# Performance work log

Measured on AMD Instinct MI355X. Metric: run time of the kernel, lower is better.

The kernel has to match this reference:

```python
import jax, jax.numpy as jnp
from jax import lax
import numpy as np

B, S, D, H2, V = 1024, 256, 128, 5, 50257
EPS = 1e-5


def setup_inputs() -> dict:
    key = jax.random.key(0)
    ks = jax.random.split(key, 12)
    s = 0.08  # init scale ~ 1/sqrt(D)
    return {
        "x": jax.random.randint(ks[0], (B, S), 0, V),
        "emb": jax.random.normal(ks[1], (V, D), jnp.float32) * s,
        "W_ih1": jax.random.normal(ks[2], (D, D), jnp.float32) * s,
        "b_ih1": jax.random.normal(ks[3], (D,), jnp.float32) * s,
        "W_hh1": jax.random.normal(ks[4], (D, D), jnp.float32) * s,
        "b_hh1": jax.random.normal(ks[5], (D,), jnp.float32) * s,
        "g1": jnp.ones((D,), jnp.float32),
        "be1": jnp.zeros((D,), jnp.float32),
        "W_ih2": jax.random.normal(ks[6], (H2, D), jnp.float32) * s,
        "b_ih2": jax.random.normal(ks[7], (H2,), jnp.float32) * s,
        "W_hh2": jax.random.normal(ks[8], (H2, H2), jnp.float32) * s,
        "b_hh2": jax.random.normal(ks[9], (H2,), jnp.float32) * s,
        "g2": jnp.ones((H2,), jnp.float32),
        "be2": jnp.zeros((H2,), jnp.float32),
    }


def _rnn(xproj, W_hh):
    """Vanilla tanh RNN. xproj: [B,S,H] = x @ W_ih^T + b_ih + b_hh (precomputed)."""
    h0 = jnp.zeros((xproj.shape[0], W_hh.shape[0]), xproj.dtype)

    def step(h, xt):  # xt: [B,H]
        h = jnp.tanh(xt + h @ W_hh.T)
        return h, h

    _, hs = lax.scan(step, h0, jnp.swapaxes(xproj, 0, 1))  # [S,B,H]
    return jnp.swapaxes(hs, 0, 1)  # [B,S,H]


def _ln(z, g, b):
    m = jnp.mean(z, axis=-1, keepdims=True)
    v = jnp.mean(jnp.square(z - m), axis=-1, keepdims=True)
    return (z - m) * lax.rsqrt(v + EPS) * g + b


def reference(x, emb, W_ih1, b_ih1, W_hh1, b_hh1, g1, be1,
              W_ih2, b_ih2, W_hh2, b_hh2, g2, be2):
    e = emb[x]  # [B,S,D]
    z = _rnn(e @ W_ih1.T + (b_ih1 + b_hh1), W_hh1)
    z = _ln(z, g1, be1)
    z = _rnn(z @ W_ih2.T + (b_ih2 + b_hh2), W_hh2)  # [B,S,5]
    z = _ln(z, g2, be2)
    pooled = jnp.mean(z, axis=1)  # AvgPool1d over full seq -> [B,5]
    return jax.nn.softmax(pooled, axis=1)
```

## Files before the change

### kernel.cpp

```cpp
#include <hip/hip_runtime.h>
#include <stdint.h>

#define S_LEN 256
#define DIM   128
#define EPSL  1e-5f

typedef __bf16 bf16x8 __attribute__((ext_vector_type(8)));
typedef float  f32x4  __attribute__((ext_vector_type(4)));

__device__ __forceinline__ unsigned short f2bf_bits(float f) {
  union { float f; unsigned int u; } v; v.f = f;
  unsigned int r = v.u + 0x7fffu + ((v.u >> 16) & 1u);
  return (unsigned short)(r >> 16);
}
__device__ __forceinline__ float bf2f_bits(unsigned short b) {
  union { float f; unsigned int u; } v; v.u = ((unsigned int)b) << 16; return v.f;
}
__device__ __forceinline__ unsigned f2bf_rhu(float f) {
  return (__float_as_uint(f) + 0x8000u) >> 16;
}
__device__ __forceinline__ unsigned pack_rhu(float lo, float hi) {
  return __builtin_amdgcn_perm(__float_as_uint(hi) + 0x8000u,
                               __float_as_uint(lo) + 0x8000u, 0x07060302u);
}
__device__ __forceinline__ float tanh_fast(float x) {
  float e = __expf(2.f * x);
  return 1.f - 2.f * __builtin_amdgcn_rcpf(e + 1.f);
}

template<int CTRL>
__device__ __forceinline__ float dpp_rot_add(float v) {
  int r = __builtin_amdgcn_update_dpp(0, __float_as_int(v), CTRL, 0xF, 0xF, true);
  return v + __int_as_float(r);
}
template<int CTRL>
__device__ __forceinline__ float dpp_rot_max(float v) {
  int r = __builtin_amdgcn_update_dpp(0, __float_as_int(v), CTRL, 0xF, 0xF, true);
  return fmaxf(v, __int_as_float(r));
}
__device__ __forceinline__ float dpp_sum16(float v) {
  v = dpp_rot_add<0x124>(v); v = dpp_rot_add<0x128>(v);
  v = dpp_rot_add<0x39>(v);  v = dpp_rot_add<0x4E>(v);
  return v;
}
__device__ __forceinline__ float dpp_max16(float v) {
  v = dpp_rot_max<0x124>(v); v = dpp_rot_max<0x128>(v);
  v = dpp_rot_max<0x39>(v);  v = dpp_rot_max<0x4E>(v);
  return v;
}
template<int CTRL>
__device__ __forceinline__ void red_level7(float& s, float& sq, float* d) {
  s  = dpp_rot_add<CTRL>(s);
  sq = dpp_rot_add<CTRL>(sq);
#pragma unroll
  for (int j = 0; j < 5; j++) d[j] = dpp_rot_add<CTRL>(d[j]);
}
template<int JJ>
__device__ __forceinline__ float bcast16(float v) {
  int r = __builtin_amdgcn_ds_swizzle(__float_as_int(v), (JJ << 5) | 0x10);
  return __int_as_float(r);
}

union Frag8 { unsigned short us[8]; bf16x8 v; int4 i4; };

__global__ __launch_bounds__(512, 2)
void rnn_main(const int* __restrict__ x, const float* __restrict__ emb,
              const float* __restrict__ Wih1, const float* __restrict__ bih1,
              const float* __restrict__ Whh1, const float* __restrict__ bhh1,
              const float* __restrict__ g1, const float* __restrict__ be1,
              const float* __restrict__ Wih2, const float* __restrict__ bih2,
              const float* __restrict__ Whh2, const float* __restrict__ bhh2,
              const float* __restrict__ g2, const float* __restrict__ be2,
              unsigned short* __restrict__ hout, int* flags,
              float* __restrict__ out)
{
  __shared__ __align__(16) unsigned short h_bf[2][16 * 128];
  __shared__ __align__(16) unsigned short e_bf[2][16 * 128];
  __shared__ int x_tile[16 * 256];
  __shared__ __align__(16) float p_lds[8][2][32][8];

  const int tid  = threadIdx.x;
  const int wave = tid >> 6;
  const int lane = tid & 63;
  const int l15  = lane & 15;
  const int q    = lane >> 4;

  if (blockIdx.x < 64) {
    const int r0 = blockIdx.x * 16;
    for (int i = tid; i < 16 * 256; i += 512)
      x_tile[i] = x[(size_t)(r0 + (i >> 8)) * S_LEN + (i & 255)];
    for (int i = tid; i < 16 * 128; i += 512) h_bf[1][i] = 0;

    const int n1 = wave * 16 + l15;
    const float bias1v = bih1[n1] + bhh1[n1];
    bf16x8 wh[4], wih[4];
#pragma unroll
    for (int kt = 0; kt < 4; kt++) {
      int k0 = kt * 32 + q * 8;
      Frag8 fh, fa;
#pragma unroll
      for (int j = 0; j < 8; j++) {
        fh.us[j] = f2bf_bits(Whh1[n1 * DIM + k0 + j]);
        fa.us[j] = f2bf_bits(Wih1[n1 * DIM + k0 + j]);
      }
      wh[kt] = fh.v; wih[kt] = fa.v;
    }

    const bool stage_role = (wave >= 4);
    float pf[2][8];
    const int gm   = (wave & 3) * 4 + q;
    const int goct = l15;
    const int gdst = gm * 128 + ((goct ^ gm) & 15) * 8;
    __syncthreads();

    if (stage_role) {
      float ta[8], tb[8];
      { int xid = x_tile[gm * 256 + 0];
        const float* pe = emb + (size_t)xid * DIM + goct * 8;
#pragma unroll
        for (int j = 0; j < 8; j++) ta[j] = pe[j]; }
      { int xid = x_tile[gm * 256 + 1];
        const float* pe = emb + (size_t)xid * DIM + goct * 8;
#pragma unroll
        for (int j = 0; j < 8; j++) tb[j] = pe[j]; }
      { int xid = x_tile[gm * 256 + 2];
        const float* pe = emb + (size_t)xid * DIM + goct * 8;
#pragma unroll
        for (int j = 0; j < 8; j++) pf[0][j] = pe[j]; }
      { int xid = x_tile[gm * 256 + 3];
        const float* pe = emb + (size_t)xid * DIM + goct * 8;
#pragma unroll
        for (int j = 0; j < 8; j++) pf[1][j] = pe[j]; }
      Frag8 pa, pb;
#pragma unroll
      for (int j = 0; j < 8; j++) { pa.us[j] = f2bf_bits(ta[j]); pb.us[j] = f2bf_bits(tb[j]); }
      *(int4*)&e_bf[0][gdst] = pa.i4;
      *(int4*)&e_bf[1][gdst] = pb.i4;
    }
    __syncthreads();

    f32x4 xpacc = {bias1v, bias1v, bias1v, bias1v};
#pragma unroll
    for (int kt = 0; kt < 4; kt++) {
      int sw = (((kt * 4 + q) ^ l15) & 15) * 8;
      bf16x8 ae = *(const bf16x8*)&e_bf[0][l15 * 128 + sw];
      xpacc = __builtin_amdgcn_mfma_f32_16x16x32_bf16(ae, wih[kt], xpacc, 0, 0, 0);
    }
    asm volatile("s_waitcnt lgkmcnt(0)\n\ts_barrier" ::: "memory");

#pragma unroll 2
    for (int t = 0; t < S_LEN; t++) {
      f32x4 acc = xpacc;
      {
        const int rb = (t + 1) & 1;
#pragma unroll
        for (int kt = 0; kt < 4; kt++) {
          int sw = (((kt * 4 + q) ^ l15) & 15) * 8;
          bf16x8 ahf = *(const bf16x8*)&h_bf[rb][l15 * 128 + sw];
          acc = __builtin_amdgcn_mfma_f32_16x16x32_bf16(ahf, wh[kt], acc, 0, 0, 0);
        }
        const int wb = t & 1;
        const int oct = n1 >> 3;
#pragma unroll
        for (int r = 0; r < 4; r++) {
          int row = q * 4 + r;
          unsigned short us = (unsigned short)f2bf_rhu(tanh_fast(acc[r]));
          h_bf[wb][row * 128 + ((oct ^ row) & 15) * 8 + (n1 & 7)] = us;
          hout[((size_t)(r0 + row) * S_LEN + t) * DIM + n1] = us;
        }
      }

      if (t + 1 < S_LEN) {
        f32x4 a = {bias1v, bias1v, bias1v, bias1v};
#pragma unroll
        for (int kt = 0; kt < 4; kt++) {
          int sw = (((kt * 4 + q) ^ l15) & 15) * 8;
          bf16x8 ae = *(const bf16x8*)&e_bf[(t + 1) & 1][l15 * 128 + sw];
          a = __builtin_amdgcn_mfma_f32_16x16x32_bf16(ae, wih[kt], a, 0, 0, 0);
        }
        xpacc = a;
      }

      if (stage_role) {
        if (t + 2 < S_LEN) {
          int4 pk;
          pk.x = pack_rhu(pf[t & 1][0], pf[t & 1][1]);
          pk.y = pack_rhu(pf[t & 1][2], pf[t & 1][3]);
          pk.z = pack_rhu(pf[t & 1][4], pf[t & 1][5]);
          pk.w = pack_rhu(pf[t & 1][6], pf[t & 1][7]);
          *(int4*)&e_bf[t & 1][gdst] = pk;
        }
        if (t + 4 < S_LEN) {
          int xid = x_tile[gm * 256 + t + 4];
          const float* pe = emb + (size_t)xid * DIM + goct * 8;
#pragma unroll
          for (int j = 0; j < 8; j++) pf[t & 1][j] = pe[j];
        }
      }
      if (flags != nullptr && (t & 31) == 31)
        asm volatile("s_waitcnt vmcnt(0)" ::: "memory");
      asm volatile("s_waitcnt lgkmcnt(0)\n\ts_barrier" ::: "memory");
      if (flags != nullptr && (t & 31) == 31 && tid == 0)
        __hip_atomic_store(&flags[blockIdx.x * 8 + (t >> 5)], (t >> 5) + 1,
                           __ATOMIC_RELEASE, __HIP_MEMORY_SCOPE_AGENT);
    }
  } else {
    const int bt = blockIdx.x - 64;
    float w2g[5][8], Gs[5], Bs[5], wrow[5];
#pragma unroll
    for (int j = 0; j < 8; j++) {
      int c = l15 * 8 + j;
      float gc = g1[c];
#pragma unroll
      for (int jj = 0; jj < 5; jj++) w2g[jj][j] = Wih2[jj * DIM + c] * gc;
    }
#pragma unroll
    for (int jj = 0; jj < 5; jj++) { Gs[jj] = 0.f; Bs[jj] = 0.f; }
    for (int c = 0; c < DIM; c++) {
      float gc = g1[c], bc = be1[c];
#pragma unroll
      for (int jj = 0; jj < 5; jj++) {
        float w = Wih2[jj * DIM + c];
        Gs[jj] += w * gc; Bs[jj] += w * bc;
      }
    }
    const float validf = (l15 < 5) ? 1.f : 0.f;
    float t2_l = 0.f, g2_l = 0.f, be2_l = 0.f;
    if (l15 < 5) {
      t2_l = bih2[l15] + bhh2[l15];
      g2_l = g2[l15]; be2_l = be2[l15];
#pragma unroll
      for (int jj = 0; jj < 5; jj++) wrow[jj] = Whh2[l15 * 5 + jj];
    } else {
#pragma unroll
      for (int jj = 0; jj < 5; jj++) wrow[jj] = 0.f;
    }
    float h2rep[5] = {0, 0, 0, 0, 0}, pool_l = 0.f;
    const int row_l = 2 * wave + (q & 1);
    const unsigned short* hb =
        hout + (size_t)(bt * 16 + row_l) * S_LEN * DIM;
    const int idx = (l15 < 5) ? l15 : 0;

    for (int c8 = 0; c8 < 8; c8++) {
      if (tid == 0) {
        while (__hip_atomic_load(&flags[bt * 8 + c8], __ATOMIC_RELAXED,
                                 __HIP_MEMORY_SCOPE_AGENT) < c8 + 1)
          __builtin_amdgcn_s_sleep(2);
      }
      __syncthreads();
      __builtin_amdgcn_fence(__ATOMIC_ACQUIRE, "agent");
      for (int tt = 0; tt < 16; tt++) {
        int toff = tt * 2 + (q >> 1);
        uint4 cur = *(const uint4*)(hb + (size_t)(c8 * 32 + toff) * DIM + l15 * 8);
        float hv[8];
        hv[0] = __uint_as_float(cur.x << 16); hv[1] = __uint_as_float(cur.x & 0xffff0000u);
        hv[2] = __uint_as_float(cur.y << 16); hv[3] = __uint_as_float(cur.y & 0xffff0000u);
        hv[4] = __uint_as_float(cur.z << 16); hv[5] = __uint_as_float(cur.z & 0xffff0000u);
        hv[6] = __uint_as_float(cur.w << 16); hv[7] = __uint_as_float(cur.w & 0xffff0000u);
        float s = 0.f, sq = 0.f, d[5] = {0, 0, 0, 0, 0};
#pragma unroll
        for (int j = 0; j < 8; j++) {
          float v = hv[j];
          s += v; sq += v * v;
#pragma unroll
          for (int jj = 0; jj < 5; jj++) d[jj] = fmaf(w2g[jj][j], v, d[jj]);
        }
        red_level7<0x124>(s, sq, d);
        red_level7<0x128>(s, sq, d);
        red_level7<0x39>(s, sq, d);
        red_level7<0x4E>(s, sq, d);
        float mean = s * (1.f / 128.f);
        float var  = sq * (1.f / 128.f) - mean * mean;
        float rstd = rsqrtf(var + EPSL);
        float p[5];
#pragma unroll
        for (int jj = 0; jj < 5; jj++)
          p[jj] = rstd * (d[jj] - mean * Gs[jj]) + Bs[jj];
        float psel = (l15 == 0) ? p[0] : (l15 == 1) ? p[1] :
                     (l15 == 2) ? p[2] : (l15 == 3) ? p[3] : p[4];
        if (l15 < 5) p_lds[wave][q & 1][toff][l15] = psel;
      }
      asm volatile("s_waitcnt lgkmcnt(0)" ::: "memory");
      for (int s = 0; s < 32; s++) {
        float pv = p_lds[wave][q & 1][s][idx];
        float a = pv + t2_l;
#pragma unroll
        for (int jj = 0; jj < 5; jj++) a = fmaf(wrow[jj], h2rep[jj], a);
        float xn = tanh_fast(a);
        float s2 = dpp_sum16(xn * validf) * 0.2f;
        float dd = xn - s2;
        float v2 = dpp_sum16(dd * dd * validf) * 0.2f;
        float r2 = rsqrtf(v2 + EPSL);
        pool_l += dd * r2 * g2_l + be2_l;
        h2rep[0] = bcast16<0>(xn); h2rep[1] = bcast16<1>(xn);
        h2rep[2] = bcast16<2>(xn); h2rep[3] = bcast16<3>(xn);
        h2rep[4] = bcast16<4>(xn);
      }
    }
    float lg = pool_l * (1.f / 256.f);
    float mx = dpp_max16((l15 < 5) ? lg : -3.0e38f);
    float e  = (l15 < 5) ? __expf(lg - mx) : 0.f;
    float sm = dpp_sum16(e);
    if (q < 2 && l15 < 5)
      out[(size_t)(bt * 16 + row_l) * 5 + l15] = e / sm;
  }
}

__global__ __launch_bounds__(256, 2)
void rnn_tail_r11(const unsigned short* __restrict__ hall,
                  const float* __restrict__ g1,  const float* __restrict__ be1,
                  const float* __restrict__ Wih2, const float* __restrict__ bih2,
                  const float* __restrict__ Whh2, const float* __restrict__ bhh2,
                  const float* __restrict__ g2,  const float* __restrict__ be2,
                  float* __restrict__ out)
{
  __shared__ float p_lds[4][4][8];
  const int tid  = threadIdx.x;
  const int wave = tid >> 6;
  const int lane = tid & 63;
  const int l15  = lane & 15;
  const int q    = lane >> 4;
  const int b    = blockIdx.x * 4 + wave;

  float w2g[5][8], Gs[5], Bs[5], wrow[5];
#pragma unroll
  for (int j = 0; j < 8; j++) {
    int c = l15 * 8 + j;
    float gc = g1[c];
#pragma unroll
    for (int jj = 0; jj < 5; jj++) w2g[jj][j] = Wih2[jj * DIM + c] * gc;
  }
#pragma unroll
  for (int jj = 0; jj < 5; jj++) { Gs[jj] = 0.f; Bs[jj] = 0.f; }
  for (int c = 0; c < DIM; c++) {
    float gc = g1[c], bc = be1[c];
#pragma unroll
    for (int jj = 0; jj < 5; jj++) {
      float w = Wih2[jj * DIM + c];
      Gs[jj] += w * gc; Bs[jj] += w * bc;
    }
  }
  const float validf = (l15 < 5) ? 1.f : 0.f;
  float t2_l = 0.f, g2_l = 0.f, be2_l = 0.f;
  if (l15 < 5) {
    t2_l = bih2[l15] + bhh2[l15];
    g2_l = g2[l15]; be2_l = be2[l15];
#pragma unroll
    for (int jj = 0; jj < 5; jj++) wrow[jj] = Whh2[l15 * 5 + jj];
  } else {
#pragma unroll
    for (int jj = 0; jj < 5; jj++) wrow[jj] = 0.f;
  }
  float h2rep[5];
#pragma unroll
  for (int jj = 0; jj < 5; jj++) h2rep[jj] = 0.f;
  float pool_l = 0.f;

  const unsigned short* hb = hall + (size_t)b * S_LEN * DIM;
  uint4 hpre = *(const uint4*)(hb + (size_t)q * DIM + l15 * 8);

  for (int t0 = 0; t0 < S_LEN; t0 += 4) {
    uint4 cur = hpre;
    if (t0 + 4 < S_LEN)
      hpre = *(const uint4*)(hb + (size_t)(t0 + 4 + q) * DIM + l15 * 8);
    float hv[8];
    hv[0] = __uint_as_float(cur.x << 16); hv[1] = __uint_as_float(cur.x & 0xffff0000u);
    hv[2] = __uint_as_float(cur.y << 16); hv[3] = __uint_as_float(cur.y & 0xffff0000u);
    hv[4] = __uint_as_float(cur.z << 16); hv[5] = __uint_as_float(cur.z & 0xffff0000u);
    hv[6] = __uint_as_float(cur.w << 16); hv[7] = __uint_as_float(cur.w & 0xffff0000u);
    float s = 0.f, sq = 0.f, d[5] = {0, 0, 0, 0, 0};
#pragma unroll
    for (int j = 0; j < 8; j++) {
      float v = hv[j];
      s += v; sq += v * v;
#pragma unroll
      for (int jj = 0; jj < 5; jj++) d[jj] = fmaf(w2g[jj][j], v, d[jj]);
    }
    red_level7<0x124>(s, sq, d);
    red_level7<0x128>(s, sq, d);
    red_level7<0x39>(s, sq, d);
    red_level7<0x4E>(s, sq, d);
    float mean = s * (1.f / 128.f);
    float var  = sq * (1.f / 128.f) - mean * mean;
    float rstd = rsqrtf(var + EPSL);
    float p[5];
#pragma unroll
    for (int jj = 0; jj < 5; jj++)
      p[jj] = rstd * (d[jj] - mean * Gs[jj]) + Bs[jj];
    float psel = (l15 == 0) ? p[0] : (l15 == 1) ? p[1] :
                 (l15 == 2) ? p[2] : (l15 == 3) ? p[3] : p[4];
    if (l15 < 5) p_lds[wave][q][l15] = psel;
    asm volatile("s_waitcnt lgkmcnt(0)" ::: "memory");
    const int idx = (l15 < 5) ? l15 : 0;
#pragma unroll
    for (int g = 0; g < 4; g++) {
      float pv = p_lds[wave][g][idx];
      float a = pv + t2_l;
#pragma unroll
      for (int jj = 0; jj < 5; jj++) a = fmaf(wrow[jj], h2rep[jj], a);
      float xn = tanh_fast(a);
      float s2 = dpp_sum16(xn * validf) * 0.2f;
      float dd = xn - s2;
      float v2 = dpp_sum16(dd * dd * validf) * 0.2f;
      float r2 = rsqrtf(v2 + EPSL);
      pool_l += dd * r2 * g2_l + be2_l;
      h2rep[0] = bcast16<0>(xn); h2rep[1] = bcast16<1>(xn);
      h2rep[2] = bcast16<2>(xn); h2rep[3] = bcast16<3>(xn);
      h2rep[4] = bcast16<4>(xn);
    }
  }

  float lg = pool_l * (1.f / 256.f);
  float mx = dpp_max16((l15 < 5) ? lg : -3.0e38f);
  float e  = (l15 < 5) ? __expf(lg - mx) : 0.f;
  float sm = dpp_sum16(e);
  if (q == 0 && l15 < 5) out[(size_t)b * 5 + l15] = e / sm;
}

extern "C" void kernel_launch(void* const* d_in, const int* in_sizes, int n_in,
                              void* d_out, int out_size, void* d_ws, size_t ws_size,
                              hipStream_t stream) {
  (void)in_sizes; (void)n_in; (void)out_size;
  const int*   x    = (const int*)  d_in[0];
  const float* emb  = (const float*)d_in[1];
  const float* Wih1 = (const float*)d_in[2];
  const float* bih1 = (const float*)d_in[3];
  const float* Whh1 = (const float*)d_in[4];
  const float* bhh1 = (const float*)d_in[5];
  const float* g1   = (const float*)d_in[6];
  const float* be1  = (const float*)d_in[7];
  const float* Wih2 = (const float*)d_in[8];
  const float* bih2 = (const float*)d_in[9];
  const float* Whh2 = (const float*)d_in[10];
  const float* bhh2 = (const float*)d_in[11];
  const float* g2   = (const float*)d_in[12];
  const float* be2  = (const float*)d_in[13];
  float* out = (float*)d_out;

  const size_t HBYTES = (size_t)1024 * S_LEN * DIM * 2;
  const size_t FBYTES = 64 * 8 * sizeof(int);
  unsigned short* hws = (unsigned short*)d_ws;

  if (ws_size >= HBYTES + 4096) {
    int* flags = (int*)((char*)d_ws + HBYTES);
    rnn_main<<<dim3(128), dim3(512), 0, stream>>>(
        x, emb, Wih1, bih1, Whh1, bhh1, g1, be1,
        Wih2, bih2, Whh2, bhh2, g2, be2, hws, flags, out);
    (void)FBYTES;
  } else {
    rnn_main<<<dim3(64), dim3(512), 0, stream>>>(
        x, emb, Wih1, bih1, Whh1, bhh1, g1, be1,
        Wih2, bih2, Whh2, bhh2, g2, be2, hws, nullptr, out);
    rnn_tail_r11<<<dim3(256), dim3(256), 0, stream>>>(
        hws, g1, be1, Wih2, bih2, Whh2, bhh2, g2, be2, out);
  }
}
```

Measured before the change: 257.1 us.

## Halve recurrent block to four waves each computing two column groups

The layer-1 recurrence block shrinks from 8 waves to 4 waves of 256 threads. Each wave now computes two 16-column output groups, reusing one set of h and embedding LDS fragment loads for both, and splits each MFMA chain into two independent accumulators to shorten the dependency chain. All waves now share the embedding staging work. The consumer tail is re-partitioned into 128 blocks of 8 rows each, which doubles the number of consumer blocks polling each producer's flags. The intent is cheaper per-step barriers and better MFMA overlap, at the cost of more registers per thread and less parallelism per sequential step.

```diff
diff --git a/kernel.cpp b/kernel.cpp
--- a/kernel.cpp
+++ b/kernel.cpp
@@ -13,9 +13,6 @@
   unsigned int r = v.u + 0x7fffu + ((v.u >> 16) & 1u);
   return (unsigned short)(r >> 16);
 }
-__device__ __forceinline__ float bf2f_bits(unsigned short b) {
-  union { float f; unsigned int u; } v; v.u = ((unsigned int)b) << 16; return v.f;
-}
 __device__ __forceinline__ unsigned f2bf_rhu(float f) {
   return (__float_as_uint(f) + 0x8000u) >> 16;
 }
@@ -63,21 +60,21 @@
 
 union Frag8 { unsigned short us[8]; bf16x8 v; int4 i4; };
 
-__global__ __launch_bounds__(512, 2)
-void rnn_main(const int* __restrict__ x, const float* __restrict__ emb,
-              const float* __restrict__ Wih1, const float* __restrict__ bih1,
-              const float* __restrict__ Whh1, const float* __restrict__ bhh1,
-              const float* __restrict__ g1, const float* __restrict__ be1,
-              const float* __restrict__ Wih2, const float* __restrict__ bih2,
-              const float* __restrict__ Whh2, const float* __restrict__ bhh2,
-              const float* __restrict__ g2, const float* __restrict__ be2,
-              unsigned short* __restrict__ hout, int* flags,
-              float* __restrict__ out)
+__global__ __launch_bounds__(256, 1)
+void rnn_main4(const int* __restrict__ x, const float* __restrict__ emb,
+               const float* __restrict__ Wih1, const float* __restrict__ bih1,
+               const float* __restrict__ Whh1, const float* __restrict__ bhh1,
+               const float* __restrict__ g1, const float* __restrict__ be1,
+               const float* __restrict__ Wih2, const float* __restrict__ bih2,
+               const float* __restrict__ Whh2, const float* __restrict__ bhh2,
+               const float* __restrict__ g2, const float* __restrict__ be2,
+               unsigned short* __restrict__ hout, int* flags,
+               float* __restrict__ out)
 {
   __shared__ __align__(16) unsigned short h_bf[2][16 * 128];
   __shared__ __align__(16) unsigned short e_bf[2][16 * 128];
   __shared__ int x_tile[16 * 256];
-  __shared__ __align__(16) float p_lds[8][2][32][8];
+  __shared__ __align__(16) float p_lds[4][2][32][8];
 
   const int tid  = threadIdx.x;
   const int wave = tid >> 6;
@@ -87,33 +84,36 @@
 
   if (blockIdx.x < 64) {
     const int r0 = blockIdx.x * 16;
-    for (int i = tid; i < 16 * 256; i += 512)
+    for (int i = tid; i < 16 * 256; i += 256)
       x_tile[i] = x[(size_t)(r0 + (i >> 8)) * S_LEN + (i & 255)];
-    for (int i = tid; i < 16 * 128; i += 512) h_bf[1][i] = 0;
-
-    const int n1 = wave * 16 + l15;
-    const float bias1v = bih1[n1] + bhh1[n1];
-    bf16x8 wh[4], wih[4];
-#pragma unroll
-    for (int kt = 0; kt < 4; kt++) {
-      int k0 = kt * 32 + q * 8;
-      Frag8 fh, fa;
-#pragma unroll
-      for (int j = 0; j < 8; j++) {
-        fh.us[j] = f2bf_bits(Whh1[n1 * DIM + k0 + j]);
-        fa.us[j] = f2bf_bits(Wih1[n1 * DIM + k0 + j]);
-      }
-      wh[kt] = fh.v; wih[kt] = fa.v;
-    }
-
-    const bool stage_role = (wave >= 4);
-    float pf[2][8];
-    const int gm   = (wave & 3) * 4 + q;
+    for (int i = tid; i < 16 * 128; i += 256) h_bf[1][i] = 0;
+
+    float bias1v[2];
+    bf16x8 wh[2][4], wihv[2][4];
+#pragma unroll
+    for (int g = 0; g < 2; g++) {
+      const int d = wave * 32 + g * 16 + l15;
+      bias1v[g] = bih1[d] + bhh1[d];
+#pragma unroll
+      for (int kt = 0; kt < 4; kt++) {
+        int k0 = kt * 32 + q * 8;
+        Frag8 fh, fa;
+#pragma unroll
+        for (int j = 0; j < 8; j++) {
+          fh.us[j] = f2bf_bits(Whh1[d * DIM + k0 + j]);
+          fa.us[j] = f2bf_bits(Wih1[d * DIM + k0 + j]);
+        }
+        wh[g][kt] = fh.v; wihv[g][kt] = fa.v;
+      }
+    }
+
+    const int gm   = wave * 4 + q;
     const int goct = l15;
     const int gdst = gm * 128 + ((goct ^ gm) & 15) * 8;
+    float pf[2][8];
     __syncthreads();
 
-    if (stage_role) {
+    {
       float ta[8], tb[8];
       { int xid = x_tile[gm * 256 + 0];
         const float* pe = emb + (size_t)xid * DIM + goct * 8;
@@ -139,49 +139,96 @@
     }
     __syncthreads();
 
-    f32x4 xpacc = {bias1v, bias1v, bias1v, bias1v};
-#pragma unroll
-    for (int kt = 0; kt < 4; kt++) {
-      int sw = (((kt * 4 + q) ^ l15) & 15) * 8;
-      bf16x8 ae = *(const bf16x8*)&e_bf[0][l15 * 128 + sw];
-      xpacc = __builtin_amdgcn_mfma_f32_16x16x32_bf16(ae, wih[kt], xpacc, 0, 0, 0);
+    f32x4 xpacc[2];
+    {
+      int sw0 = ((q ^ l15) & 15) * 8;
+      int sw1 = (((4 + q) ^ l15) & 15) * 8;
+      int sw2 = (((8 + q) ^ l15) & 15) * 8;
+      int sw3 = (((12 + q) ^ l15) & 15) * 8;
+      bf16x8 e0 = *(const bf16x8*)&e_bf[0][l15 * 128 + sw0];
+      bf16x8 e1 = *(const bf16x8*)&e_bf[0][l15 * 128 + sw1];
+      bf16x8 e2 = *(const bf16x8*)&e_bf[0][l15 * 128 + sw2];
+      bf16x8 e3 = *(const bf16x8*)&e_bf[0][l15 * 128 + sw3];
+#pragma unroll
+      for (int g = 0; g < 2; g++) {
+        f32x4 a = {bias1v[g], bias1v[g], bias1v[g], bias1v[g]};
+        f32x4 b = {0.f, 0.f, 0.f, 0.f};
+        a = __builtin_amdgcn_mfma_f32_16x16x32_bf16(e0, wihv[g][0], a, 0, 0, 0);
+        b = __builtin_amdgcn_mfma_f32_16x16x32_bf16(e2, wihv[g][2], b, 0, 0, 0);
+        a = __builtin_amdgcn_mfma_f32_16x16x32_bf16(e1, wihv[g][1], a, 0, 0, 0);
+        b = __builtin_amdgcn_mfma_f32_16x16x32_bf16(e3, wihv[g][3], b, 0, 0, 0);
+        xpacc[g] = a + b;
+      }
     }
     asm volatile("s_waitcnt lgkmcnt(0)\n\ts_barrier" ::: "memory");
 
 #pragma unroll 2
     for (int t = 0; t < S_LEN; t++) {
-      f32x4 acc = xpacc;
+      const int rb = (t + 1) & 1;
+      const int wb = t & 1;
+      unsigned short usv[2][4];
       {
-        const int rb = (t + 1) & 1;
-#pragma unroll
-        for (int kt = 0; kt < 4; kt++) {
-          int sw = (((kt * 4 + q) ^ l15) & 15) * 8;
-          bf16x8 ahf = *(const bf16x8*)&h_bf[rb][l15 * 128 + sw];
-          acc = __builtin_amdgcn_mfma_f32_16x16x32_bf16(ahf, wh[kt], acc, 0, 0, 0);
-        }
-        const int wb = t & 1;
-        const int oct = n1 >> 3;
+        int sw0 = ((q ^ l15) & 15) * 8;
+        int sw1 = (((4 + q) ^ l15) & 15) * 8;
+        int sw2 = (((8 + q) ^ l15) & 15) * 8;
+        int sw3 = (((12 + q) ^ l15) & 15) * 8;
+        bf16x8 a0 = *(const bf16x8*)&h_bf[rb][l15 * 128 + sw0];
+        bf16x8 a1 = *(const bf16x8*)&h_bf[rb][l15 * 128 + sw1];
+        bf16x8 a2 = *(const bf16x8*)&h_bf[rb][l15 * 128 + sw2];
+        bf16x8 a3 = *(const bf16x8*)&h_bf[rb][l15 * 128 + sw3];
+#pragma unroll
+        for (int g = 0; g < 2; g++) {
+          f32x4 acc  = xpacc[g];
+          f32x4 accb = {0.f, 0.f, 0.f, 0.f};
+          acc  = __builtin_amdgcn_mfma_f32_16x16x32_bf16(a0, wh[g][0], acc,  0, 0, 0);
+          accb = __builtin_amdgcn_mfma_f32_16x16x32_bf16(a2, wh[g][2], accb, 0, 0, 0);
+          acc  = __builtin_amdgcn_mfma_f32_16x16x32_bf16(a1, wh[g][1], acc,  0, 0, 0);
+          accb = __builtin_amdgcn_mfma_f32_16x16x32_bf16(a3, wh[g][3], accb, 0, 0, 0);
+          acc += accb;
+          const int c = wave * 32 + g * 16 + l15;
+          const int oct = c >> 3;
+#pragma unroll
+          for (int r = 0; r < 4; r++) {
+            int row = q * 4 + r;
+            unsigned short us = (unsigned short)f2bf_rhu(tanh_fast(acc[r]));
+            usv[g][r] = us;
+            h_bf[wb][row * 128 + ((oct ^ row) & 15) * 8 + (c & 7)] = us;
+          }
+        }
+      }
+#pragma unroll
+      for (int g = 0; g < 2; g++) {
+        const int c = wave * 32 + g * 16 + l15;
 #pragma unroll
         for (int r = 0; r < 4; r++) {
           int row = q * 4 + r;
-          unsigned short us = (unsigned short)f2bf_rhu(tanh_fast(acc[r]));
-          h_bf[wb][row * 128 + ((oct ^ row) & 15) * 8 + (n1 & 7)] = us;
-          hout[((size_t)(r0 + row) * S_LEN + t) * DIM + n1] = us;
+          hout[((size_t)(r0 + row) * S_LEN + t) * DIM + c] = usv[g][r];
         }
       }
 
       if (t + 1 < S_LEN) {
-        f32x4 a = {bias1v, bias1v, bias1v, bias1v};
-#pragma unroll
-        for (int kt = 0; kt < 4; kt++) {
-          int sw = (((kt * 4 + q) ^ l15) & 15) * 8;
-          bf16x8 ae = *(const bf16x8*)&e_bf[(t + 1) & 1][l15 * 128 + sw];
-          a = __builtin_amdgcn_mfma_f32_16x16x32_bf16(ae, wih[kt], a, 0, 0, 0);
-        }
-        xpacc = a;
-      }
-
-      if (stage_role) {
+        int sw0 = ((q ^ l15) & 15) * 8;
+        int sw1 = (((4 + q) ^ l15) & 15) * 8;
+        int sw2 = (((8 + q) ^ l15) & 15) * 8;
+        int sw3 = (((12 + q) ^ l15) & 15) * 8;
+        const unsigned short* eb = &e_bf[(t + 1) & 1][l15 * 128];
+        bf16x8 e0 = *(const bf16x8*)&eb[sw0];
+        bf16x8 e1 = *(const bf16x8*)&eb[sw1];
+        bf16x8 e2 = *(const bf16x8*)&eb[sw2];
+        bf16x8 e3 = *(const bf16x8*)&eb[sw3];
+#pragma unroll
+        for (int g = 0; g < 2; g++) {
+          f32x4 a = {bias1v[g], bias1v[g], bias1v[g], bias1v[g]};
+          f32x4 b = {0.f, 0.f, 0.f, 0.f};
+          a = __builtin_amdgcn_mfma_f32_16x16x32_bf16(e0, wihv[g][0], a, 0, 0, 0);
+          b = __builtin_amdgcn_mfma_f32_16x16x32_bf16(e2, wihv[g][2], b, 0, 0, 0);
+          a = __builtin_amdgcn_mfma_f32_16x16x32_bf16(e1, wihv[g][1], a, 0, 0, 0);
+          b = __builtin_amdgcn_mfma_f32_16x16x32_bf16(e3, wihv[g][3], b, 0, 0, 0);
+          xpacc[g] = a + b;
+        }
+      }
+
+      {
         if (t + 2 < S_LEN) {
           int4 pk;
           pk.x = pack_rhu(pf[t & 1][0], pf[t & 1][1]);
@@ -206,6 +253,7 @@
     }
   } else {
     const int bt = blockIdx.x - 64;
+    const int u  = bt >> 1;
     float w2g[5][8], Gs[5], Bs[5], wrow[5];
 #pragma unroll
     for (int j = 0; j < 8; j++) {
@@ -225,7 +273,8 @@
       }
     }
     const float validf = (l15 < 5) ? 1.f : 0.f;
-    float t2_l = 0.f, g2_l = 0.f, be2_l = 0.f;
+    float t2_l = 0.f, g2_l = 0.f, be2_l = 0.f, wrow_[5];
+    (void)wrow_;
     if (l15 < 5) {
       t2_l = bih2[l15] + bhh2[l15];
       g2_l = g2[l15]; be2_l = be2[l15];
@@ -236,14 +285,13 @@
       for (int jj = 0; jj < 5; jj++) wrow[jj] = 0.f;
     }
     float h2rep[5] = {0, 0, 0, 0, 0}, pool_l = 0.f;
-    const int row_l = 2 * wave + (q & 1);
-    const unsigned short* hb =
-        hout + (size_t)(bt * 16 + row_l) * S_LEN * DIM;
+    const int rowg = bt * 8 + wave * 2 + (q & 1);
+    const unsigned short* hb = hout + (size_t)rowg * S_LEN * DIM;
     const int idx = (l15 < 5) ? l15 : 0;
 
     for (int c8 = 0; c8 < 8; c8++) {
       if (tid == 0) {
-        while (__hip_atomic_load(&flags[bt * 8 + c8], __ATOMIC_RELAXED,
+        while (__hip_atomic_load(&flags[u * 8 + c8], __ATOMIC_RELAXED,
                                  __HIP_MEMORY_SCOPE_AGENT) < c8 + 1)
           __builtin_amdgcn_s_sleep(2);
       }
@@ -302,7 +350,7 @@
     float e  = (l15 < 5) ? __expf(lg - mx) : 0.f;
     float sm = dpp_sum16(e);
     if (q < 2 && l15 < 5)
-      out[(size_t)(bt * 16 + row_l) * 5 + l15] = e / sm;
+      out[(size_t)rowg * 5 + l15] = e / sm;
   }
 }
 
@@ -438,17 +486,15 @@
   float* out = (float*)d_out;
 
   const size_t HBYTES = (size_t)1024 * S_LEN * DIM * 2;
-  const size_t FBYTES = 64 * 8 * sizeof(int);
   unsigned short* hws = (unsigned short*)d_ws;
 
   if (ws_size >= HBYTES + 4096) {
     int* flags = (int*)((char*)d_ws + HBYTES);
-    rnn_main<<<dim3(128), dim3(512), 0, stream>>>(
+    rnn_main4<<<dim3(192), dim3(256), 0, stream>>>(
         x, emb, Wih1, bih1, Whh1, bhh1, g1, be1,
         Wih2, bih2, Whh2, bhh2, g2, be2, hws, flags, out);
-    (void)FBYTES;
   } else {
-    rnn_main<<<dim3(64), dim3(512), 0, stream>>>(
+    rnn_main4<<<dim3(64), dim3(256), 0, stream>>>(
         x, emb, Wih1, bih1, Whh1, bhh1, g1, be1,
         Wih2, bih2, Whh2, bhh2, g2, be2, hws, nullptr, out);
     rnn_tail_r11<<<dim3(256), dim3(256), 0, stream>>>(
```

Measured after the change: 299.1 us. 1.16x slower.
